# Optimization experiments

Hardware: AMD Instinct MI355X
Metric: run time of the kernel (lower is better)

Reference implementation:

```python
import jax, jax.numpy as jnp
import numpy as np

HEIGHT = 480
K = 16
RADIUS = 5.0 / HEIGHT


def ball_query_idx(xy, radius, k):
    """pytorch3d-style ball_query on 2D points (t-channel is zeroed in the
    original, so 3D distance == 2D distance on (x, y)).
    Returns first-k (in point-index order) neighbor indices within radius;
    slots with no neighbor are filled with the query's own index (the
    module's `-1 -> self` replacement).  xy: [B, N, 2] -> idx: [B, N, k] int32."""
    B, N, _ = xy.shape
    sq = jnp.sum(xy * xy, axis=-1)  # [B, N]
    # d2[b, i, j] = ||xy[b,i] - xy[b,j]||^2, via GEMM (no [B,N,N,2] intermediate)
    d2 = sq[:, :, None] + sq[:, None, :] - 2.0 * jnp.einsum('bnd,bmd->bnm', xy, xy)
    within = d2 < radius * radius  # [B, N, N]
    ar = jnp.arange(N, dtype=jnp.int32)
    # key = j if within else N; k smallest keys == first k neighbors in index order
    keys = jnp.where(within, ar[None, None, :], N)
    neg_top, _ = jax.lax.top_k(-keys, k)  # k smallest keys, ascending after negate
    idx = -neg_top  # [B, N, k]
    self_idx = jnp.broadcast_to(ar[None, :, None], (B, N, k))
    return jnp.where(idx < N, idx, self_idx)


def knn_gather(x, idx):
    # x: [B, N, D], idx: [B, N, k] -> [B, N, k, D]
    return jax.vmap(lambda xb, ib: xb[ib])(x, idx)


def setup_inputs() -> dict:
    key = jax.random.key(0)
    k1, k2, k3 = jax.random.split(key, 3)
    B, N = 8, 4096
    out_ch = 64
    hid = out_ch * 2          # 128
    in_ch = K * 2             # 32
    xytp = jax.random.uniform(k1, (B, N, 4), dtype=jnp.float32)
    W1 = jax.random.normal(k2, (in_ch, hid), dtype=jnp.float32) / np.sqrt(in_ch)
    b1 = jnp.zeros((hid,), dtype=jnp.float32)
    W2 = jax.random.normal(k3, (hid, out_ch), dtype=jnp.float32) / np.sqrt(hid)
    b2 = jnp.zeros((out_ch,), dtype=jnp.float32)
    return {"xytp": xytp, "W1": W1, "b1": b1, "W2": W2, "b2": b2}


def reference(xytp, W1, b1, W2, b2):
    xy = xytp[..., 1:3]  # [B, N, 2]
    # ball query runs on detached coords in the original
    idx = ball_query_idx(jax.lax.stop_gradient(xy), RADIUS, K)  # [B, N, K]
    delta = xy[:, :, None, :] - knn_gather(xy, idx)  # [B, N, K, 2]
    B, N = delta.shape[:2]
    emb = delta.reshape(B, N, K * 2)  # [B, N, 2K]
    h = jax.nn.relu(emb @ W1 + b1)
    return h @ W2 + b2  # [B, N, out_channel]
```

## Files before the change

kernel.cpp:

```cpp
#include <hip/hip_runtime.h>

#define NB    8
#define NPTS  4096
#define KNN   16
#define GRID  64
#define NCELL (GRID * GRID)
#define CAP   16

#define POISON ((int)0xAAAAAAAAu)

#define R2F ((float)((5.0 / 480.0) * (5.0 / 480.0)))


#define WS_BUCKET 0x20000

__global__ __launch_bounds__(256) void k_bucket(
    const float4* __restrict__ xytp4, int* __restrict__ cnts,
    float4* __restrict__ bucket) {
#pragma clang fp contract(off)
  int g = blockIdx.x * 256 + threadIdx.x;
  int b = g >> 12, n = g & 4095;
  float4 P = xytp4[g];
  float x = P.y, y = P.z;
  float sq = x * x + y * y;
  int cx = min(GRID - 1, max(0, (int)(x * (float)GRID)));
  int cy = min(GRID - 1, max(0, (int)(y * (float)GRID)));
  int cell = b * NCELL + cy * GRID + cx;
  int pos = atomicAdd(&cnts[cell], 1) - POISON;
  if (pos >= 0 && pos < CAP)
    bucket[cell * CAP + pos] = make_float4(x, y, sq, __int_as_float(n));
}

__global__ __launch_bounds__(1024, 8) void k_qmlp(
    const float4* __restrict__ xytp4, const int* __restrict__ cnts,
    const float4* __restrict__ bucket, const float* __restrict__ W1,
    const float* __restrict__ b1, const float* __restrict__ W2,
    const float* __restrict__ b2, float* __restrict__ out) {
#pragma clang fp contract(off)
  __shared__ float qx[64], qy[64], qsq[64];
  __shared__ unsigned short lists[64 * 9 * CAP];
  __shared__ int cnt9[64 * 9];
  __shared__ unsigned short scand[64 * 24];
  __shared__ unsigned short idxls[64 * KNN];
  __shared__ __align__(16) float embs[64 * 36];
  __shared__ __align__(16) float hs[64 * 132];

  const int t = threadIdx.x;
  const int p = t & 63;
  const int qq = t >> 6;
  const int pbase = blockIdx.x * 64;
  const int bb = pbase & ~4095;
  const int b = pbase >> 12;

  if (t < 64) {
    float4 P = xytp4[pbase + t];
    float x = P.y, y = P.z;
    qx[t] = x; qy[t] = y;
    qsq[t] = x * x + y * y;
  }
  if (t < 64 * 9) cnt9[t] = 0;
  __syncthreads();

  if (qq < 9) {
    float xn = qx[p], yn = qy[p], sqn = qsq[p];
    int cx = min(GRID - 1, max(0, (int)(xn * (float)GRID)));
    int cy = min(GRID - 1, max(0, (int)(yn * (float)GRID)));
    int row = cy + (qq / 3) - 1;
    int col = cx + (qq % 3) - 1;
    if (row >= 0 && row < GRID && col >= 0 && col < GRID) {
      int cell = b * NCELL + row * GRID + col;
      int cnt = min(max(cnts[cell] - POISON, 0), CAP);
      const float4* bk = bucket + cell * CAP;
      unsigned short* lst = &lists[(p * 9 + qq) * CAP];
      int c = 0;
      for (int i = 0; i < cnt; ++i) {
        float4 Q = bk[i];
        float tt = fmaf(yn, Q.y, xn * Q.x);
        float d = (sqn + Q.z) - (tt + tt);
        if (d < R2F) lst[c++] = (unsigned short)__float_as_int(Q.w);
      }
      cnt9[p * 9 + qq] = c;
    }
  }
  __syncthreads();

  if (t < 64) {
    unsigned short* cand = &scand[t * 24];
    int c = 0;
    for (int cc = 0; cc < 9; ++cc) {
      int rc = cnt9[t * 9 + cc];
      const unsigned short* lp = &lists[(t * 9 + cc) * CAP];
      for (int j = 0; j < rc && c < 24; ++j) cand[c++] = lp[j];
    }
    for (int i = 1; i < c; ++i) {
      unsigned short key = cand[i];
      int j = i - 1;
      while (j >= 0 && cand[j] > key) { cand[j + 1] = cand[j]; --j; }
      cand[j + 1] = key;
    }
    if (c > KNN) c = KNN;
    unsigned short selfI = (unsigned short)((pbase + t) & 4095);
    for (int k = 0; k < KNN; ++k)
      idxls[t * KNN + k] = (k < c) ? cand[k] : selfI;
  }
  __syncthreads();

  {
    int m = idxls[p * KNN + qq];
    float4 M = xytp4[bb + m];
    embs[p * 36 + 2 * qq] = qx[p] - M.y;
    embs[p * 36 + 2 * qq + 1] = qy[p] - M.z;
  }
  __syncthreads();

  {
    const int u0 = __builtin_amdgcn_readfirstlane(qq) * 8;
    float h[8];
#pragma unroll
    for (int j = 0; j < 8; ++j) h[j] = b1[u0 + j];
    const float4* er = (const float4*)&embs[p * 36];
#pragma unroll
    for (int g = 0; g < 8; ++g) {
      float4 e4 = er[g];
      const float* __restrict__ w0 = W1 + (4 * g) * 128 + u0;
#pragma unroll
      for (int j = 0; j < 8; ++j) h[j] = fmaf(e4.x, w0[j], h[j]);
#pragma unroll
      for (int j = 0; j < 8; ++j) h[j] = fmaf(e4.y, w0[128 + j], h[j]);
#pragma unroll
      for (int j = 0; j < 8; ++j) h[j] = fmaf(e4.z, w0[256 + j], h[j]);
#pragma unroll
      for (int j = 0; j < 8; ++j) h[j] = fmaf(e4.w, w0[384 + j], h[j]);
    }
    float* hr = &hs[p * 132 + u0];
    ((float4*)hr)[0] = make_float4(fmaxf(h[0], 0.f), fmaxf(h[1], 0.f),
                                   fmaxf(h[2], 0.f), fmaxf(h[3], 0.f));
    ((float4*)hr)[1] = make_float4(fmaxf(h[4], 0.f), fmaxf(h[5], 0.f),
                                   fmaxf(h[6], 0.f), fmaxf(h[7], 0.f));
  }
  __syncthreads();

  {
    const int o0 = __builtin_amdgcn_readfirstlane(qq) * 4;
    float acc[4];
#pragma unroll
    for (int j = 0; j < 4; ++j) acc[j] = b2[o0 + j];
    const float4* hv4 = (const float4*)&hs[p * 132];
#pragma unroll 4
    for (int g = 0; g < 32; ++g) {
      float4 hv = hv4[g];
      const float* __restrict__ w0 = W2 + (4 * g) * 64 + o0;
#pragma unroll
      for (int j = 0; j < 4; ++j) acc[j] = fmaf(hv.x, w0[j], acc[j]);
#pragma unroll
      for (int j = 0; j < 4; ++j) acc[j] = fmaf(hv.y, w0[64 + j], acc[j]);
#pragma unroll
      for (int j = 0; j < 4; ++j) acc[j] = fmaf(hv.z, w0[128 + j], acc[j]);
#pragma unroll
      for (int j = 0; j < 4; ++j) acc[j] = fmaf(hv.w, w0[192 + j], acc[j]);
    }
    *(float4*)(out + (size_t)(pbase + p) * 64 + o0) =
        make_float4(acc[0], acc[1], acc[2], acc[3]);
  }
}

extern "C" void kernel_launch(void* const* d_in, const int* in_sizes, int n_in,
                              void* d_out, int out_size, void* d_ws, size_t ws_size,
                              hipStream_t stream) {
  const float4* xytp4 = (const float4*)d_in[0];
  const float* W1 = (const float*)d_in[1];
  const float* b1 = (const float*)d_in[2];
  const float* W2 = (const float*)d_in[3];
  const float* b2 = (const float*)d_in[4];
  float* out = (float*)d_out;

  char* ws = (char*)d_ws;
  int* cnts = (int*)ws;
  float4* bucket = (float4*)(ws + WS_BUCKET);

  hipLaunchKernelGGL(k_bucket, dim3(128), dim3(256), 0, stream, xytp4, cnts,
                     bucket);
  hipLaunchKernelGGL(k_qmlp, dim3(512), dim3(1024), 0, stream, xytp4, cnts,
                     bucket, W1, b1, W2, b2, out);
}
```

Baseline: 88.94 us.

## Split ball query into separate per-point kernel writing packed indices

Moves the neighbor search out of the fused query+MLP kernel into a new kernel where each thread handles one query point. It scans its 3x3 cells, sorts candidates and writes 16 packed 16-bit indices to workspace. The MLP kernel then just loads those indices, which removes the 9-way split, the shared list buffers and two barriers. The cost is an extra kernel launch and a global round-trip for the indices. The query kernel also runs only 256 blocks of 128 threads with a per-thread local array, so its occupancy is low.

```diff
diff --git a/kernel.cpp b/kernel.cpp
--- a/kernel.cpp
+++ b/kernel.cpp
@@ -13,6 +13,7 @@
 
 
 #define WS_BUCKET 0x20000
+#define WS_IDX    0x820000
 
 __global__ __launch_bounds__(256) void k_bucket(
     const float4* __restrict__ xytp4, int* __restrict__ cnts,
@@ -31,17 +32,60 @@
     bucket[cell * CAP + pos] = make_float4(x, y, sq, __int_as_float(n));
 }
 
-__global__ __launch_bounds__(1024, 8) void k_qmlp(
+__global__ __launch_bounds__(128) void k_query(
     const float4* __restrict__ xytp4, const int* __restrict__ cnts,
-    const float4* __restrict__ bucket, const float* __restrict__ W1,
-    const float* __restrict__ b1, const float* __restrict__ W2,
-    const float* __restrict__ b2, float* __restrict__ out) {
+    const float4* __restrict__ bucket, uint4* __restrict__ idxw) {
 #pragma clang fp contract(off)
-  __shared__ float qx[64], qy[64], qsq[64];
-  __shared__ unsigned short lists[64 * 9 * CAP];
-  __shared__ int cnt9[64 * 9];
-  __shared__ unsigned short scand[64 * 24];
-  __shared__ unsigned short idxls[64 * KNN];
+  int g = blockIdx.x * 128 + threadIdx.x;
+  int b = g >> 12, n = g & 4095;
+  float4 P = xytp4[g];
+  float xn = P.y, yn = P.z;
+  float sqn = xn * xn + yn * yn;
+  int cx = min(GRID - 1, max(0, (int)(xn * (float)GRID)));
+  int cy = min(GRID - 1, max(0, (int)(yn * (float)GRID)));
+  int r0 = max(cy - 1, 0), r1 = min(cy + 1, GRID - 1);
+  int c0 = max(cx - 1, 0), c1 = min(cx + 1, GRID - 1);
+  unsigned short cand[24];
+  int c = 0;
+  for (int row = r0; row <= r1; ++row) {
+    for (int col = c0; col <= c1; ++col) {
+      int cell = b * NCELL + row * GRID + col;
+      int cnt = min(max(cnts[cell] - POISON, 0), CAP);
+      const float4* bk = bucket + cell * CAP;
+      for (int i = 0; i < cnt; ++i) {
+        float4 Q = bk[i];
+        float tt = fmaf(yn, Q.y, xn * Q.x);
+        float d = (sqn + Q.z) - (tt + tt);
+        if (d < R2F && c < 24) cand[c++] = (unsigned short)__float_as_int(Q.w);
+      }
+    }
+  }
+  for (int i = 1; i < c; ++i) {
+    unsigned short key = cand[i];
+    int j = i - 1;
+    while (j >= 0 && cand[j] > key) { cand[j + 1] = cand[j]; --j; }
+    cand[j + 1] = key;
+  }
+  if (c > KNN) c = KNN;
+  unsigned v[8];
+#pragma unroll
+  for (int h = 0; h < 8; ++h) {
+    unsigned lo = (2 * h < c) ? cand[2 * h] : (unsigned)n;
+    unsigned hi = (2 * h + 1 < c) ? cand[2 * h + 1] : (unsigned)n;
+    v[h] = lo | (hi << 16);
+  }
+  idxw[g * 2] = make_uint4(v[0], v[1], v[2], v[3]);
+  idxw[g * 2 + 1] = make_uint4(v[4], v[5], v[6], v[7]);
+}
+
+__global__ __launch_bounds__(1024, 8) void k_mlp(
+    const float4* __restrict__ xytp4, const uint4* __restrict__ idxw,
+    const float* __restrict__ W1, const float* __restrict__ b1,
+    const float* __restrict__ W2, const float* __restrict__ b2,
+    float* __restrict__ out) {
+#pragma clang fp contract(off)
+  __shared__ float qx[64], qy[64];
+  __shared__ __align__(16) unsigned short idxls[64 * KNN];
   __shared__ __align__(16) float embs[64 * 36];
   __shared__ __align__(16) float hs[64 * 132];
 
@@ -50,58 +94,11 @@
   const int qq = t >> 6;
   const int pbase = blockIdx.x * 64;
   const int bb = pbase & ~4095;
-  const int b = pbase >> 12;
 
+  if (t < 128) ((uint4*)idxls)[t] = idxw[blockIdx.x * 128 + t];
   if (t < 64) {
     float4 P = xytp4[pbase + t];
-    float x = P.y, y = P.z;
-    qx[t] = x; qy[t] = y;
-    qsq[t] = x * x + y * y;
-  }
-  if (t < 64 * 9) cnt9[t] = 0;
-  __syncthreads();
-
-  if (qq < 9) {
-    float xn = qx[p], yn = qy[p], sqn = qsq[p];
-    int cx = min(GRID - 1, max(0, (int)(xn * (float)GRID)));
-    int cy = min(GRID - 1, max(0, (int)(yn * (float)GRID)));
-    int row = cy + (qq / 3) - 1;
-    int col = cx + (qq % 3) - 1;
-    if (row >= 0 && row < GRID && col >= 0 && col < GRID) {
-      int cell = b * NCELL + row * GRID + col;
-      int cnt = min(max(cnts[cell] - POISON, 0), CAP);
-      const float4* bk = bucket + cell * CAP;
-      unsigned short* lst = &lists[(p * 9 + qq) * CAP];
-      int c = 0;
-      for (int i = 0; i < cnt; ++i) {
-        float4 Q = bk[i];
-        float tt = fmaf(yn, Q.y, xn * Q.x);
-        float d = (sqn + Q.z) - (tt + tt);
-        if (d < R2F) lst[c++] = (unsigned short)__float_as_int(Q.w);
-      }
-      cnt9[p * 9 + qq] = c;
-    }
-  }
-  __syncthreads();
-
-  if (t < 64) {
-    unsigned short* cand = &scand[t * 24];
-    int c = 0;
-    for (int cc = 0; cc < 9; ++cc) {
-      int rc = cnt9[t * 9 + cc];
-      const unsigned short* lp = &lists[(t * 9 + cc) * CAP];
-      for (int j = 0; j < rc && c < 24; ++j) cand[c++] = lp[j];
-    }
-    for (int i = 1; i < c; ++i) {
-      unsigned short key = cand[i];
-      int j = i - 1;
-      while (j >= 0 && cand[j] > key) { cand[j + 1] = cand[j]; --j; }
-      cand[j + 1] = key;
-    }
-    if (c > KNN) c = KNN;
-    unsigned short selfI = (unsigned short)((pbase + t) & 4095);
-    for (int k = 0; k < KNN; ++k)
-      idxls[t * KNN + k] = (k < c) ? cand[k] : selfI;
+    qx[t] = P.y; qy[t] = P.z;
   }
   __syncthreads();
 
@@ -177,9 +174,12 @@
   char* ws = (char*)d_ws;
   int* cnts = (int*)ws;
   float4* bucket = (float4*)(ws + WS_BUCKET);
+  uint4* idxw = (uint4*)(ws + WS_IDX);
 
   hipLaunchKernelGGL(k_bucket, dim3(128), dim3(256), 0, stream, xytp4, cnts,
                      bucket);
-  hipLaunchKernelGGL(k_qmlp, dim3(512), dim3(1024), 0, stream, xytp4, cnts,
-                     bucket, W1, b1, W2, b2, out);
+  hipLaunchKernelGGL(k_query, dim3(256), dim3(128), 0, stream, xytp4, cnts,
+                     bucket, idxw);
+  hipLaunchKernelGGL(k_mlp, dim3(512), dim3(1024), 0, stream, xytp4, idxw, W1,
+                     b1, W2, b2, out);
 }
```

Result: slower. 110.8 us (+24.6%).

## Halve query-MLP block to 512 threads with doubled per-thread work

Applied to the files above, without the earlier changes.

Shrinks the fused query+MLP block from 1024 to 512 threads. Each thread now covers more neighbor cells in the grid scan, more embedding gather slots, and twice as many hidden and output columns in the two MLP layers. The shared query-coordinate staging and its barrier are dropped; query points are reloaded from global memory instead. This cuts idle threads and one sync, at the cost of more registers per thread and redundant query loads.

```diff
diff --git a/kernel.cpp b/kernel.cpp
--- a/kernel.cpp
+++ b/kernel.cpp
@@ -31,13 +31,12 @@
     bucket[cell * CAP + pos] = make_float4(x, y, sq, __int_as_float(n));
 }
 
-__global__ __launch_bounds__(1024, 8) void k_qmlp(
+__global__ __launch_bounds__(512, 4) void k_qmlp(
     const float4* __restrict__ xytp4, const int* __restrict__ cnts,
     const float4* __restrict__ bucket, const float* __restrict__ W1,
     const float* __restrict__ b1, const float* __restrict__ W2,
     const float* __restrict__ b2, float* __restrict__ out) {
 #pragma clang fp contract(off)
-  __shared__ float qx[64], qy[64], qsq[64];
   __shared__ unsigned short lists[64 * 9 * CAP];
   __shared__ int cnt9[64 * 9];
   __shared__ unsigned short scand[64 * 24];
@@ -52,34 +51,29 @@
   const int bb = pbase & ~4095;
   const int b = pbase >> 12;
 
-  if (t < 64) {
-    float4 P = xytp4[pbase + t];
-    float x = P.y, y = P.z;
-    qx[t] = x; qy[t] = y;
-    qsq[t] = x * x + y * y;
-  }
-  if (t < 64 * 9) cnt9[t] = 0;
-  __syncthreads();
-
-  if (qq < 9) {
-    float xn = qx[p], yn = qy[p], sqn = qsq[p];
+  {
+    float4 Pq = xytp4[pbase + p];
+    float xn = Pq.y, yn = Pq.z;
+    float sqn = xn * xn + yn * yn;
     int cx = min(GRID - 1, max(0, (int)(xn * (float)GRID)));
     int cy = min(GRID - 1, max(0, (int)(yn * (float)GRID)));
-    int row = cy + (qq / 3) - 1;
-    int col = cx + (qq % 3) - 1;
-    if (row >= 0 && row < GRID && col >= 0 && col < GRID) {
-      int cell = b * NCELL + row * GRID + col;
-      int cnt = min(max(cnts[cell] - POISON, 0), CAP);
-      const float4* bk = bucket + cell * CAP;
-      unsigned short* lst = &lists[(p * 9 + qq) * CAP];
+    for (int c9 = qq; c9 < 9; c9 += 8) {
+      int row = cy + (c9 / 3) - 1;
+      int col = cx + (c9 % 3) - 1;
       int c = 0;
-      for (int i = 0; i < cnt; ++i) {
-        float4 Q = bk[i];
-        float tt = fmaf(yn, Q.y, xn * Q.x);
-        float d = (sqn + Q.z) - (tt + tt);
-        if (d < R2F) lst[c++] = (unsigned short)__float_as_int(Q.w);
+      if (row >= 0 && row < GRID && col >= 0 && col < GRID) {
+        int cell = b * NCELL + row * GRID + col;
+        int cnt = min(max(cnts[cell] - POISON, 0), CAP);
+        const float4* bk = bucket + cell * CAP;
+        unsigned short* lst = &lists[(p * 9 + c9) * CAP];
+        for (int i = 0; i < cnt; ++i) {
+          float4 Q = bk[i];
+          float tt = fmaf(yn, Q.y, xn * Q.x);
+          float d = (sqn + Q.z) - (tt + tt);
+          if (d < R2F) lst[c++] = (unsigned short)__float_as_int(Q.w);
+        }
       }
-      cnt9[p * 9 + qq] = c;
+      cnt9[p * 9 + c9] = c;
     }
   }
   __syncthreads();
@@ -105,62 +99,66 @@
   }
   __syncthreads();
 
-  {
-    int m = idxls[p * KNN + qq];
+  for (int s = t; s < 64 * KNN; s += 512) {
+    int pp = s >> 4, kk = s & 15;
+    float4 Pq = xytp4[pbase + pp];
+    int m = idxls[s];
     float4 M = xytp4[bb + m];
-    embs[p * 36 + 2 * qq] = qx[p] - M.y;
-    embs[p * 36 + 2 * qq + 1] = qy[p] - M.z;
+    embs[pp * 36 + 2 * kk] = Pq.y - M.y;
+    embs[pp * 36 + 2 * kk + 1] = Pq.z - M.z;
   }
   __syncthreads();
 
   {
-    const int u0 = __builtin_amdgcn_readfirstlane(qq) * 8;
-    float h[8];
+    const int u0 = __builtin_amdgcn_readfirstlane(qq) * 16;
+    float h[16];
 #pragma unroll
-    for (int j = 0; j < 8; ++j) h[j] = b1[u0 + j];
+    for (int j = 0; j < 16; ++j) h[j] = b1[u0 + j];
     const float4* er = (const float4*)&embs[p * 36];
 #pragma unroll
     for (int g = 0; g < 8; ++g) {
       float4 e4 = er[g];
       const float* __restrict__ w0 = W1 + (4 * g) * 128 + u0;
 #pragma unroll
-      for (int j = 0; j < 8; ++j) h[j] = fmaf(e4.x, w0[j], h[j]);
+      for (int j = 0; j < 16; ++j) h[j] = fmaf(e4.x, w0[j], h[j]);
 #pragma unroll
-      for (int j = 0; j < 8; ++j) h[j] = fmaf(e4.y, w0[128 + j], h[j]);
+      for (int j = 0; j < 16; ++j) h[j] = fmaf(e4.y, w0[128 + j], h[j]);
 #pragma unroll
-      for (int j = 0; j < 8; ++j) h[j] = fmaf(e4.z, w0[256 + j], h[j]);
+      for (int j = 0; j < 16; ++j) h[j] = fmaf(e4.z, w0[256 + j], h[j]);
 #pragma unroll
-      for (int j = 0; j < 8; ++j) h[j] = fmaf(e4.w, w0[384 + j], h[j]);
+      for (int j = 0; j < 16; ++j) h[j] = fmaf(e4.w, w0[384 + j], h[j]);
     }
     float* hr = &hs[p * 132 + u0];
-    ((float4*)hr)[0] = make_float4(fmaxf(h[0], 0.f), fmaxf(h[1], 0.f),
-                                   fmaxf(h[2], 0.f), fmaxf(h[3], 0.f));
-    ((float4*)hr)[1] = make_float4(fmaxf(h[4], 0.f), fmaxf(h[5], 0.f),
-                                   fmaxf(h[6], 0.f), fmaxf(h[7], 0.f));
+#pragma unroll
+    for (int j4 = 0; j4 < 4; ++j4)
+      ((float4*)hr)[j4] = make_float4(
+          fmaxf(h[4 * j4], 0.f), fmaxf(h[4 * j4 + 1], 0.f),
+          fmaxf(h[4 * j4 + 2], 0.f), fmaxf(h[4 * j4 + 3], 0.f));
   }
   __syncthreads();
 
   {
-    const int o0 = __builtin_amdgcn_readfirstlane(qq) * 4;
-    float acc[4];
+    const int o0 = __builtin_amdgcn_readfirstlane(qq) * 8;
+    float acc[8];
 #pragma unroll
-    for (int j = 0; j < 4; ++j) acc[j] = b2[o0 + j];
+    for (int j = 0; j < 8; ++j) acc[j] = b2[o0 + j];
     const float4* hv4 = (const float4*)&hs[p * 132];
-#pragma unroll 4
+#pragma unroll 8
     for (int g = 0; g < 32; ++g) {
       float4 hv = hv4[g];
       const float* __restrict__ w0 = W2 + (4 * g) * 64 + o0;
 #pragma unroll
-      for (int j = 0; j < 4; ++j) acc[j] = fmaf(hv.x, w0[j], acc[j]);
+      for (int j = 0; j < 8; ++j) acc[j] = fmaf(hv.x, w0[j], acc[j]);
 #pragma unroll
-      for (int j = 0; j < 4; ++j) acc[j] = fmaf(hv.y, w0[64 + j], acc[j]);
+      for (int j = 0; j < 8; ++j) acc[j] = fmaf(hv.y, w0[64 + j], acc[j]);
 #pragma unroll
-      for (int j = 0; j < 4; ++j) acc[j] = fmaf(hv.z, w0[128 + j], acc[j]);
+      for (int j = 0; j < 8; ++j) acc[j] = fmaf(hv.z, w0[128 + j], acc[j]);
 #pragma unroll
-      for (int j = 0; j < 4; ++j) acc[j] = fmaf(hv.w, w0[192 + j], acc[j]);
+      for (int j = 0; j < 8; ++j) acc[j] = fmaf(hv.w, w0[192 + j], acc[j]);
     }
-    *(float4*)(out + (size_t)(pbase + p) * 64 + o0) =
-        make_float4(acc[0], acc[1], acc[2], acc[3]);
+    float* op = out + (size_t)(pbase + p) * 64 + o0;
+    *(float4*)op = make_float4(acc[0], acc[1], acc[2], acc[3]);
+    *(float4*)(op + 4) = make_float4(acc[4], acc[5], acc[6], acc[7]);
   }
 }
 
@@ -180,6 +178,6 @@
 
   hipLaunchKernelGGL(k_bucket, dim3(128), dim3(256), 0, stream, xytp4, cnts,
                      bucket);
-  hipLaunchKernelGGL(k_qmlp, dim3(512), dim3(1024), 0, stream, xytp4, cnts,
+  hipLaunchKernelGGL(k_qmlp, dim3(512), dim3(512), 0, stream, xytp4, cnts,
                      bucket, W1, b1, W2, b2, out);
 }
```

Result: no change. 89.14 us (+0.2%).
